# Kernel tuning notes

Hardware: AMD Instinct MI355X
Metric: run time of the kernel (lower is better)

## Reference

```python
import jax, jax.numpy as jnp
import numpy as np

SEQ, BATCH, IN, HID = 2048, 4096, 4, 3


def setup_inputs() -> dict:
    key = jax.random.key(0)
    ks = jax.random.split(key, 6)
    s = 1.0 / np.sqrt(HID)  # PyTorch RNN init scale
    return {
        "x": jax.random.normal(ks[0], (SEQ, BATCH, IN), dtype=jnp.float32),
        "h0": jax.random.normal(ks[1], (1, BATCH, HID), dtype=jnp.float32),
        "W_ih": jax.random.uniform(ks[2], (HID, IN), minval=-s, maxval=s, dtype=jnp.float32),
        "W_hh": jax.random.uniform(ks[3], (HID, HID), minval=-s, maxval=s, dtype=jnp.float32),
        "b_ih": jax.random.uniform(ks[4], (HID,), minval=-s, maxval=s, dtype=jnp.float32),
        "b_hh": jax.random.uniform(ks[5], (HID,), minval=-s, maxval=s, dtype=jnp.float32),
    }


def reference(x, h0, W_ih, W_hh, b_ih, b_hh):
    # Single-layer ReLU RNN (batch_first=False):
    #   h_t = relu(x_t @ W_ih^T + b_ih + h_{t-1} @ W_hh^T + b_hh)
    # Precompute the input projection for all timesteps (vectorized GEMM),
    # then scan only the tiny recurrent update.
    pre = jnp.einsum('tbi,hi->tbh', x, W_ih) + b_ih + b_hh  # [T,B,H]

    def step(h, pre_t):
        h_new = jax.nn.relu(pre_t + h @ W_hh.T)  # [B,H]
        return h_new, h_new

    h_last, outs = jax.lax.scan(step, h0[0], pre)
    return outs, h_last[None]  # ([T,B,H], [1,B,H]) as nn.RNN returns
```

## Files before the change

### kernel.cpp

```cpp
#include <hip/hip_runtime.h>

#define T_SEQ  2048
#define BATCH  4096
#define CHUNK  8
#define NCHUNK (T_SEQ / CHUNK)
#define XR     8
#define PR     4
#define XLOOK  6
#define NITER  (NCHUNK + 2)

typedef float v4f __attribute__((ext_vector_type(4)));
struct Out3 { float a, b, c; };

#define AS1c(p) ((const __attribute__((address_space(1))) void*)(p))
#define AS3(p)  ((__attribute__((address_space(3))) void*)(p))

#define BARRIER() do {                      \
    __builtin_amdgcn_sched_barrier(0);      \
    __builtin_amdgcn_s_barrier();           \
    __builtin_amdgcn_sched_barrier(0);      \
} while (0)

__global__ __launch_bounds__(192, 1) void rnn_fused(
    const float* __restrict__ x,
    const float* __restrict__ h0,
    const float* __restrict__ Wih,
    const float* __restrict__ Whh,
    const float* __restrict__ bih,
    const float* __restrict__ bhh,
    float* __restrict__ out)
{
    __shared__ v4f xs[XR * CHUNK * 64];
    __shared__ v4f ps[PR * CHUNK * 64];

    const int tid  = threadIdx.x;
    const int lane = tid & 63;
    const int wid  = tid >> 6;
    const int b    = blockIdx.x * 64 + lane;

    const v4f* __restrict__ xg = (const v4f*)x;

#define STAGE(c) do {                                                          \
        const int _s0 = ((c) & (XR - 1)) * CHUNK;                              \
        _Pragma("unroll")                                                      \
        for (int _u = 0; _u < CHUNK; ++_u) {                                   \
            __builtin_amdgcn_global_load_lds(                                  \
                AS1c(xg + (size_t)((c) * CHUNK + _u) * BATCH + b),             \
                AS3(&xs[(_s0 + _u) * 64]), 16, 0, 0);                          \
        }                                                                      \
    } while (0)

    if (wid == 2) {
        for (int c = 0; c < XLOOK; ++c) STAGE(c);
#pragma unroll 1
        for (int i = 0; i < NITER; ++i) {
            if (i + XLOOK < NCHUNK) STAGE(i + XLOOK);
            asm volatile("s_waitcnt vmcnt(48)" ::: "memory");
            BARRIER();
        }
    } else if (wid == 1) {
        const float w00 = Wih[0], w01 = Wih[1], w02 = Wih[2],  w03 = Wih[3];
        const float w10 = Wih[4], w11 = Wih[5], w12 = Wih[6],  w13 = Wih[7];
        const float w20 = Wih[8], w21 = Wih[9], w22 = Wih[10], w23 = Wih[11];
        const float bb0 = bih[0] + bhh[0];
        const float bb1 = bih[1] + bhh[1];
        const float bb2 = bih[2] + bhh[2];
#pragma unroll 1
        for (int i = 0; i < NITER; ++i) {
            const int ci = i - 1;
            if (ci >= 0 && ci < NCHUNK) {
                const v4f* __restrict__ xr = &xs[((ci & (XR - 1)) * CHUNK) * 64 + lane];
                v4f* __restrict__ pw = &ps[((ci & (PR - 1)) * CHUNK) * 64 + lane];
#pragma unroll
                for (int u = 0; u < CHUNK; ++u) {
                    v4f xv = xr[u * 64];
                    float p0 = fmaf(w00, xv.x, fmaf(w01, xv.y,
                               fmaf(w02, xv.z, fmaf(w03, xv.w, bb0))));
                    float p1 = fmaf(w10, xv.x, fmaf(w11, xv.y,
                               fmaf(w12, xv.z, fmaf(w13, xv.w, bb1))));
                    float p2 = fmaf(w20, xv.x, fmaf(w21, xv.y,
                               fmaf(w22, xv.z, fmaf(w23, xv.w, bb2))));
                    v4f pv; pv.x = p0; pv.y = p1; pv.z = p2; pv.w = 0.0f;
                    pw[u * 64] = pv;
                }
            }
            asm volatile("s_waitcnt lgkmcnt(0)" ::: "memory");
            BARRIER();
        }
    } else {
        const float a00 = Whh[0], a01 = Whh[1], a02 = Whh[2];
        const float a10 = Whh[3], a11 = Whh[4], a12 = Whh[5];
        const float a20 = Whh[6], a21 = Whh[7], a22 = Whh[8];
        float h0r = h0[b * 3 + 0];
        float h1r = h0[b * 3 + 1];
        float h2r = h0[b * 3 + 2];
        Out3* __restrict__ ob = (Out3*)out;
#pragma unroll 1
        for (int i = 0; i < NITER; ++i) {
            const int cj = i - 2;
            if (cj >= 0) {
                const v4f* __restrict__ pr = &ps[((cj & (PR - 1)) * CHUNK) * 64 + lane];
                Out3* __restrict__ obase = ob + (size_t)cj * CHUNK * BATCH + b;
#pragma unroll
                for (int u = 0; u < CHUNK; ++u) {
                    v4f pv = pr[u * 64];
                    float t0 = fmaf(a00, h0r, fmaf(a01, h1r, fmaf(a02, h2r, pv.x)));
                    float t1 = fmaf(a10, h0r, fmaf(a11, h1r, fmaf(a12, h2r, pv.y)));
                    float t2 = fmaf(a20, h0r, fmaf(a21, h1r, fmaf(a22, h2r, pv.z)));
                    h0r = fmaxf(t0, 0.0f);
                    h1r = fmaxf(t1, 0.0f);
                    h2r = fmaxf(t2, 0.0f);
                    obase[(size_t)u * BATCH] = Out3{h0r, h1r, h2r};
                }
            }
            BARRIER();
        }
        Out3* lastp = (Out3*)(out + (size_t)T_SEQ * BATCH * 3);
        lastp[b] = Out3{h0r, h1r, h2r};
    }
#undef STAGE
}

extern "C" void kernel_launch(void* const* d_in, const int* in_sizes, int n_in,
                              void* d_out, int out_size, void* d_ws, size_t ws_size,
                              hipStream_t stream) {
    const float* x   = (const float*)d_in[0];
    const float* h0  = (const float*)d_in[1];
    const float* Wih = (const float*)d_in[2];
    const float* Whh = (const float*)d_in[3];
    const float* bih = (const float*)d_in[4];
    const float* bhh = (const float*)d_in[5];
    float* out = (float*)d_out;

    rnn_fused<<<BATCH / 64, 192, 0, stream>>>(x, h0, Wih, Whh, bih, bhh, out);
}
```

Measured before the change: 285.7 us.

## Spread x staging across six loader waves with doubled chunk size

Replaces the single loader wave with six loader waves (512 threads) that stage chunks round-robin. Each wave issues one chunk four iterations ahead and waits with vmcnt(0) only for its own chunk. Chunk size doubles to 16 timesteps, which halves the number of block barriers, and the x and p ring buffers are resized to 6 and 2 slots. The aim is more memory-level parallelism on the x loads and less per-wave vmcnt serialization, at the cost of more waves per block and larger LDS use.

Result: faster. 263.8 us (-7.7%).

```diff
diff --git a/kernel.cpp b/kernel.cpp
--- a/kernel.cpp
+++ b/kernel.cpp
@@ -2,11 +2,12 @@
 
 #define T_SEQ  2048
 #define BATCH  4096
-#define CHUNK  8
+#define CHUNK  16
 #define NCHUNK (T_SEQ / CHUNK)
-#define XR     8
-#define PR     4
-#define XLOOK  6
+#define XR     6
+#define PR     2
+#define NS     6
+#define LOOK   4
 #define NITER  (NCHUNK + 2)
 
 typedef float v4f __attribute__((ext_vector_type(4)));
@@ -15,13 +16,13 @@
 #define AS1c(p) ((const __attribute__((address_space(1))) void*)(p))
 #define AS3(p)  ((__attribute__((address_space(3))) void*)(p))
 
-#define BARRIER() do {                      \
-    __builtin_amdgcn_sched_barrier(0);      \
-    __builtin_amdgcn_s_barrier();           \
-    __builtin_amdgcn_sched_barrier(0);      \
+#define BARRIER() do {                              \
+    __builtin_amdgcn_sched_barrier(0);              \
+    asm volatile("s_barrier" ::: "memory");         \
+    __builtin_amdgcn_sched_barrier(0);              \
 } while (0)
 
-__global__ __launch_bounds__(192, 1) void rnn_fused(
+__global__ __launch_bounds__(512, 1) void rnn_fused(
     const float* __restrict__ x,
     const float* __restrict__ h0,
     const float* __restrict__ Wih,
@@ -41,7 +42,7 @@
     const v4f* __restrict__ xg = (const v4f*)x;
 
 #define STAGE(c) do {                                                          \
-        const int _s0 = ((c) & (XR - 1)) * CHUNK;                              \
+        const int _s0 = ((c) % XR) * CHUNK;                                    \
         _Pragma("unroll")                                                      \
         for (int _u = 0; _u < CHUNK; ++_u) {                                   \
             __builtin_amdgcn_global_load_lds(                                  \
@@ -50,12 +51,18 @@
         }                                                                      \
     } while (0)
 
-    if (wid == 2) {
-        for (int c = 0; c < XLOOK; ++c) STAGE(c);
+    if (wid >= 2) {
+        const int s = wid - 2;
+        if (s < LOOK) STAGE(s);
+        int nstage = (s < LOOK) ? (s + NS) : s;
+        int nwait  = s;
 #pragma unroll 1
         for (int i = 0; i < NITER; ++i) {
-            if (i + XLOOK < NCHUNK) STAGE(i + XLOOK);
-            asm volatile("s_waitcnt vmcnt(48)" ::: "memory");
+            if (nstage < NCHUNK && i + LOOK == nstage) { STAGE(nstage); nstage += NS; }
+            if (i == nwait) {
+                asm volatile("s_waitcnt vmcnt(0)" ::: "memory");
+                nwait += NS;
+            }
             BARRIER();
         }
     } else if (wid == 1) {
@@ -67,10 +74,10 @@
         const float bb2 = bih[2] + bhh[2];
 #pragma unroll 1
         for (int i = 0; i < NITER; ++i) {
-            const int ci = i - 1;
-            if (ci >= 0 && ci < NCHUNK) {
-                const v4f* __restrict__ xr = &xs[((ci & (XR - 1)) * CHUNK) * 64 + lane];
-                v4f* __restrict__ pw = &ps[((ci & (PR - 1)) * CHUNK) * 64 + lane];
+            const int cp = i - 1;
+            if (cp >= 0 && cp < NCHUNK) {
+                const v4f* __restrict__ xr = &xs[((cp % XR) * CHUNK) * 64 + lane];
+                v4f* __restrict__ pw = &ps[((cp & (PR - 1)) * CHUNK) * 64 + lane];
 #pragma unroll
                 for (int u = 0; u < CHUNK; ++u) {
                     v4f xv = xr[u * 64];
@@ -83,8 +90,8 @@
                     v4f pv; pv.x = p0; pv.y = p1; pv.z = p2; pv.w = 0.0f;
                     pw[u * 64] = pv;
                 }
+                asm volatile("s_waitcnt lgkmcnt(0)" ::: "memory");
             }
-            asm volatile("s_waitcnt lgkmcnt(0)" ::: "memory");
             BARRIER();
         }
     } else {
@@ -97,10 +104,10 @@
         Out3* __restrict__ ob = (Out3*)out;
 #pragma unroll 1
         for (int i = 0; i < NITER; ++i) {
-            const int cj = i - 2;
-            if (cj >= 0) {
-                const v4f* __restrict__ pr = &ps[((cj & (PR - 1)) * CHUNK) * 64 + lane];
-                Out3* __restrict__ obase = ob + (size_t)cj * CHUNK * BATCH + b;
+            const int cc = i - 2;
+            if (cc >= 0) {
+                const v4f* __restrict__ pr = &ps[((cc & (PR - 1)) * CHUNK) * 64 + lane];
+                Out3* __restrict__ obase = ob + (size_t)cc * CHUNK * BATCH + b;
 #pragma unroll
                 for (int u = 0; u < CHUNK; ++u) {
                     v4f pv = pr[u * 64];
@@ -132,5 +139,5 @@
     const float* bhh = (const float*)d_in[5];
     float* out = (float*)d_out;
 
-    rnn_fused<<<BATCH / 64, 192, 0, stream>>>(x, h0, Wih, Whh, bih, bhh, out);
+    rnn_fused<<<BATCH / 64, 512, 0, stream>>>(x, h0, Wih, Whh, bih, bhh, out);
 }
```
